# Performance work log

Hardware: AMD Instinct MI355X
Metric: run time of the kernel (lower is better)

Reference implementation:

```python
import jax, jax.numpy as jnp
import numpy as np

V = 20000          # vocab size ('ALL')
E = 512            # embedding_dim
H = 1024           # rnn_hidden_size
LD = 256           # latent_dim
NL = 2             # num_rnn_layers_dec (hidden_factor = 2, unidirectional)
B = 32
S = 256
PAD = 0
CUT0 = 30          # cutoffs = [30, 100, 1000], div_value = 4.0
TAIL_SPECS = [(30, 100, 256), (100, 1000, 64), (1000, V, 16)]  # (low, high, proj_dim)


def setup_inputs() -> dict:
    key = jax.random.key(0)
    ks = jax.random.split(key, 24)
    w = lambda k, shp: (0.02 * jax.random.normal(k, shp)).astype(jnp.float32)

    z = jax.random.normal(ks[0], (B, LD), dtype=jnp.float32)
    emb = w(ks[1], (V, E))
    l2h_w = w(ks[2], (NL * H, LD))
    l2h_b = jnp.zeros((NL * H,), jnp.float32)
    # RNN layer 0 (input E) and layer 1 (input H)
    rnn0_wih = w(ks[3], (H, E)); rnn0_whh = w(ks[4], (H, H))
    rnn0_bih = jnp.zeros((H,), jnp.float32); rnn0_bhh = jnp.zeros((H,), jnp.float32)
    rnn1_wih = w(ks[5], (H, H)); rnn1_whh = w(ks[6], (H, H))
    rnn1_bih = jnp.zeros((H,), jnp.float32); rnn1_bhh = jnp.zeros((H,), jnp.float32)
    # adaptive softmax: head = 30 shortlist + 3 cluster logits
    head_w = w(ks[7], (CUT0 + 3, H))
    tail_p0 = w(ks[8], (256, H));  tail_w0 = w(ks[9], (70, 256))
    tail_p1 = w(ks[10], (64, H));  tail_w1 = w(ks[11], (900, 64))
    tail_p2 = w(ks[12], (16, H));  tail_w2 = w(ks[13], (V - 1000, 16))

    length = jax.random.randint(ks[14], (B,), 32, S + 1)
    pos = jnp.arange(S)[None, :]
    mask = pos < length[:, None]
    inp_seq = jax.random.randint(ks[15], (B, S), 4, V)
    inp_seq = jnp.where(mask, inp_seq, PAD)
    target_seq = jax.random.randint(ks[16], (B, S), 4, V)
    target_seq = jnp.where(mask, target_seq, PAD)

    return dict(z=z, emb=emb, l2h_w=l2h_w, l2h_b=l2h_b,
                rnn0_wih=rnn0_wih, rnn0_whh=rnn0_whh, rnn0_bih=rnn0_bih, rnn0_bhh=rnn0_bhh,
                rnn1_wih=rnn1_wih, rnn1_whh=rnn1_whh, rnn1_bih=rnn1_bih, rnn1_bhh=rnn1_bhh,
                head_w=head_w, tail_p0=tail_p0, tail_w0=tail_w0, tail_p1=tail_p1,
                tail_w1=tail_w1, tail_p2=tail_p2, tail_w2=tail_w2,
                inp_seq=inp_seq, target_seq=target_seq, length=length)


def _rnn_layer(x, h0, wih, whh, bih, bhh):
    # x: [B,S,D], h0: [B,H] -> [B,S,H]  (tanh vanilla RNN)
    def step(h, xt):
        h = jnp.tanh(xt @ wih.T + bih + h @ whh.T + bhh)
        return h, h
    _, ys = jax.lax.scan(step, h0, jnp.swapaxes(x, 0, 1))
    return jnp.swapaxes(ys, 0, 1)


def _adaptive_log_prob(x, head_w, tails):
    # x: [N,H] -> full log-probs [N,V] (AdaptiveLogSoftmaxWithLoss.log_prob)
    head_lp = jax.nn.log_softmax(x @ head_w.T, axis=-1)  # [N, 33]
    parts = [head_lp[:, :CUT0]]
    for i, (p, w) in enumerate(tails):
        clp = jax.nn.log_softmax((x @ p.T) @ w.T, axis=-1)
        parts.append(clp + head_lp[:, CUT0 + i][:, None])
    return jnp.concatenate(parts, axis=1)


def reference(z, emb, l2h_w, l2h_b,
              rnn0_wih, rnn0_whh, rnn0_bih, rnn0_bhh,
              rnn1_wih, rnn1_whh, rnn1_bih, rnn1_bhh,
              head_w, tail_p0, tail_w0, tail_p1, tail_w1, tail_p2, tail_w2,
              inp_seq, target_seq, length):
    # sort inputs by descending length (hidden is NOT sorted, as in the original)
    sorted_idx = jnp.argsort(-length)
    x = emb[inp_seq[sorted_idx]]                         # [B,S,E]
    hid = z @ l2h_w.T + l2h_b                            # [B, 2H]
    hidden = hid.reshape(NL, B, H)                       # torch .view(hidden_factor, B, H)
    h1 = _rnn_layer(x, hidden[0], rnn0_wih, rnn0_whh, rnn0_bih, rnn0_bhh)
    h2 = _rnn_layer(h1, hidden[1], rnn1_wih, rnn1_whh, rnn1_bih, rnn1_bhh)
    rev = jnp.argsort(sorted_idx)
    out = h2[rev].reshape(-1, H)                         # [N,H]
    tgt = target_seq.reshape(-1)                         # [N]
    lp = _adaptive_log_prob(out, head_w,
                            [(tail_p0, tail_w0), (tail_p1, tail_w1), (tail_p2, tail_w2)])
    nll = -jnp.take_along_axis(lp, tgt[:, None], axis=1)[:, 0]
    nll = jnp.where(tgt == PAD, 0.0, nll)
    return jnp.sum(nll)
```

## Files before the change

### kernel.cpp

```cpp
#include <hip/hip_runtime.h>
#include <hip/hip_bf16.h>
#include <math.h>

#define BB 32
#define SS 256
#define EE 512
#define HH 1024
#define LDM 256
#define NROW (BB*SS)
#define NWG 64

typedef __attribute__((ext_vector_type(8))) short bf16x8;
typedef __attribute__((ext_vector_type(4))) float f32x4;
typedef unsigned long long u64;

static __device__ inline unsigned short f2bf(float f){
  unsigned u = __float_as_uint(f);
  unsigned r = (u + 0x7fffu + ((u >> 16) & 1u)) >> 16;
  return (unsigned short)r;
}
static __device__ inline unsigned short f2bf_fast(float f){
  return (unsigned short)((__float_as_uint(f) + 0x8000u) >> 16);
}
static __device__ inline bf16x8 cvt8(float4 x, float4 y){
  union { ushort s[8]; bf16x8 v; } t;
  t.s[0]=f2bf_fast(x.x); t.s[1]=f2bf_fast(x.y); t.s[2]=f2bf_fast(x.z); t.s[3]=f2bf_fast(x.w);
  t.s[4]=f2bf_fast(y.x); t.s[5]=f2bf_fast(y.y); t.s[6]=f2bf_fast(y.z); t.s[7]=f2bf_fast(y.w);
  return t.v;
}
static __device__ inline unsigned packbf(float a, float b){
  return (unsigned)f2bf(a) | ((unsigned)f2bf(b) << 16);
}

static __device__ inline float ftanh(float x){
  float e = __expf(2.f*x);
  return 1.f - 2.f/(e + 1.f);
}

#define GLD(dst, p) asm volatile("global_load_dwordx4 %0, %1, off sc0 sc1" \
                                 : "=v"(dst) : "v"(p) : "memory")

static __device__ inline bf16x8 asbf(f32x4 x){
  union { f32x4 f; bf16x8 b; } u; u.f = x; return u.b;
}

__global__ void k_sort(const int* __restrict__ length, int* __restrict__ sorted_idx){
  int b = threadIdx.x;
  if (b >= BB) return;
  int lb = length[b];
  int r = 0;
  for (int o = 0; o < BB; ++o){
    int lo = length[o];
    if (lo > lb || (lo == lb && o < b)) ++r;
  }
  sorted_idx[r] = b;
}

__global__ void k_maps(const int* __restrict__ sorted_idx,
                       const int* __restrict__ inp_seq, const int* __restrict__ tgt_seq,
                       int* __restrict__ tokmap, int* __restrict__ tgtmap){
  int bs = blockIdx.x; int t = threadIdx.x;
  int b = sorted_idx[bs];
  tokmap[bs*SS + t] = inp_seq[b*SS + t];
  tgtmap[bs*SS + t] = tgt_seq[b*SS + t];
}

__global__ __launch_bounds__(256) void k_hid(const float* __restrict__ z,
        const float* __restrict__ w, const float* __restrict__ bias,
        ushort* __restrict__ hb0){
  int id = blockIdx.x*256 + threadIdx.x;
  int b = id >> 11, c = id & 2047;
  const float4* zr = (const float4*)(z + b*LDM);
  const float4* wr = (const float4*)(w + (size_t)c*LDM);
  float a0=0,a1=0,a2=0,a3=0;
  #pragma unroll 4
  for (int k=0;k<LDM/4;k++){ float4 zz=zr[k], ww=wr[k];
    a0+=zz.x*ww.x; a1+=zz.y*ww.y; a2+=zz.z*ww.z; a3+=zz.w*ww.w; }
  float val = a0+a1+a2+a3 + bias[c];
  int layer = id >> 15, bp = (id >> 10) & 31, j = id & 1023;
  hb0[(layer<<15) + ((j>>3)<<8) + (bp<<3) + (j&7)] = f2bf(val);
}

__global__ __launch_bounds__(256) void k_gemm_bf16(
    const float* __restrict__ A, int lda, const int* __restrict__ rowmap,
    const float* __restrict__ Bm,
    const float* __restrict__ bias0, const float* __restrict__ bias1,
    float* __restrict__ C, int M, int N, int K)
{
  __shared__ ushort As[128*72];
  __shared__ ushort Bs[128*72];
  const int nt = blockIdx.x * 128, mt = blockIdx.y * 128;
  const int tid = threadIdx.x;
  const int wv = tid >> 6, ln = tid & 63;
  const int wm = wv & 1, wn = wv >> 1;
  const int lc = ln & 15, quad = ln >> 4;
  f32x4 acc[4][4] = {{{0.f,0.f,0.f,0.f}}};

  for (int s = 0; s < K; s += 64){
    __syncthreads();
    #pragma unroll
    for (int cc = 0; cc < 4; ++cc){
      int ch = tid*4 + cc;
      int r = ch >> 3, c = ch & 7;
      int ar = mt + r;
      const float* ap = A + (size_t)(rowmap ? rowmap[ar] : ar)*lda + s + c*8;
      float4 x = *(const float4*)ap, y = *(const float4*)(ap+4);
      *(bf16x8*)&As[r*72 + c*8] = cvt8(x, y);
      int br = nt + r; if (br >= N) br = N - 1;
      const float* bp = Bm + (size_t)br*K + s + c*8;
      float4 bx = *(const float4*)bp, by = *(const float4*)(bp+4);
      *(bf16x8*)&Bs[r*72 + c*8] = cvt8(bx, by);
    }
    __syncthreads();
    #pragma unroll
    for (int kq = 0; kq < 2; ++kq){
      int cq = kq*4 + quad;
      bf16x8 af[4], bfv[4];
      #pragma unroll
      for (int i=0;i<4;i++) af[i]  = *(const bf16x8*)&As[(wm*64 + i*16 + lc)*72 + cq*8];
      #pragma unroll
      for (int j=0;j<4;j++) bfv[j] = *(const bf16x8*)&Bs[(wn*64 + j*16 + lc)*72 + cq*8];
      #pragma unroll
      for (int i=0;i<4;i++)
        #pragma unroll
        for (int j=0;j<4;j++)
          acc[i][j] = __builtin_amdgcn_mfma_f32_16x16x32_bf16(af[i], bfv[j], acc[i][j], 0, 0, 0);
    }
  }
  #pragma unroll
  for (int j=0;j<4;j++){
    int col = nt + wn*64 + j*16 + lc;
    if (col < N){
      float badd = (bias0 ? bias0[col] : 0.f) + (bias1 ? bias1[col] : 0.f);
      #pragma unroll
      for (int i=0;i<4;i++){
        int row = mt + wm*64 + i*16 + quad*4;
        #pragma unroll
        for (int r=0;r<4;r++)
          C[(size_t)(row+r)*N + col] = acc[i][j][r] + badd;
      }
    }
  }
}

__global__ __launch_bounds__(256, 1) void k_rnn_fused(
    const float* __restrict__ pre0, float* __restrict__ h2out,
    const float* __restrict__ w0hh, const float* __restrict__ w1ih,
    const float* __restrict__ w1hh,
    const float* __restrict__ b1ih, const float* __restrict__ b1hh,
    const ushort* __restrict__ hb0, ushort* __restrict__ hx, int* ctr)
{
  __shared__ ushort w0F[16384], wiF[16384], whF[16384];
  __shared__ float red[4352];
  const int wg  = blockIdx.x;
  const int tid = threadIdx.x;
  const int j0  = wg * 16;

  for (int c = tid; c < 4096; c += 256){
    int rr = c >> 8, cc = (c & 255) * 4;
    int dst = ((cc >> 3)*16 + rr)*8 + (cc & 7);
    size_t srow = (size_t)(j0 + rr)*HH + cc;
    float4 w4; uint2 p;
    w4 = *(const float4*)&w0hh[srow];
    p.x = packbf(w4.x, w4.y); p.y = packbf(w4.z, w4.w);
    *(uint2*)&w0F[dst] = p;
    w4 = *(const float4*)&w1ih[srow];
    p.x = packbf(w4.x, w4.y); p.y = packbf(w4.z, w4.w);
    *(uint2*)&wiF[dst] = p;
    w4 = *(const float4*)&w1hh[srow];
    p.x = packbf(w4.x, w4.y); p.y = packbf(w4.z, w4.w);
    *(uint2*)&whF[dst] = p;
  }
  const int lane = tid & 63, wv = tid >> 6;
  const int col = lane & 15, quad = lane >> 4;
  const int ob = tid >> 3, oj = (tid << 1) & 15;

  float2 pre = *(const float2*)&pre0[((size_t)ob*SS + 0)*HH + j0 + oj];
  float2 pre2;
  pre2.x = b1ih[j0+oj]   + b1hh[j0+oj];
  pre2.y = b1ih[j0+oj+1] + b1hh[j0+oj+1];
  __syncthreads();

  for (int r = 0; r < SS; ++r){
    const u64* s1 = (const u64*)(r == 0 ? hb0 : hx + ((r-1)&1)*32768);
    const u64* s2 = (r == 0) ? (const u64*)hb0
                  : (const u64*)(r == 1 ? hb0 + 32768 : hx + (2 + (r&1))*32768);
    f32x4 a0r[8], a1r[8], c0r[8], c1r[8];
    #pragma unroll
    for (int ks = 0; ks < 8; ++ks){
      int kb = wv*32 + ks*4 + quad;
      const u64* p = s1 + (kb << 6) + (col << 1);
      GLD(a0r[ks], p);
      GLD(a1r[ks], p + 32);
    }
    if (r > 0){
      #pragma unroll
      for (int ks = 0; ks < 8; ++ks){
        int kb = wv*32 + ks*4 + quad;
        const u64* p = s2 + (kb << 6) + (col << 1);
        GLD(c0r[ks], p);
        GLD(c1r[ks], p + 32);
      }
    }
    asm volatile("s_waitcnt vmcnt(0)" ::: "memory");
    __builtin_amdgcn_sched_barrier(0);

    f32x4 accA0 = {0.f,0.f,0.f,0.f}, accA1 = {0.f,0.f,0.f,0.f};
    f32x4 accB0 = {0.f,0.f,0.f,0.f}, accB1 = {0.f,0.f,0.f,0.f};
    #pragma unroll
    for (int ks = 0; ks < 8; ++ks){
      int kb = wv*32 + ks*4 + quad;
      bf16x8 b0 = *(const bf16x8*)&w0F[(kb*16 + col)*8];
      accA0 = __builtin_amdgcn_mfma_f32_16x16x32_bf16(asbf(a0r[ks]), b0, accA0, 0, 0, 0);
      accA1 = __builtin_amdgcn_mfma_f32_16x16x32_bf16(asbf(a1r[ks]), b0, accA1, 0, 0, 0);
      bf16x8 bi = *(const bf16x8*)&wiF[(kb*16 + col)*8];
      accB0 = __builtin_amdgcn_mfma_f32_16x16x32_bf16(asbf(a0r[ks]), bi, accB0, 0, 0, 0);
      accB1 = __builtin_amdgcn_mfma_f32_16x16x32_bf16(asbf(a1r[ks]), bi, accB1, 0, 0, 0);
    }
    if (r > 0){
      #pragma unroll
      for (int ks = 0; ks < 8; ++ks){
        int kb = wv*32 + ks*4 + quad;
        bf16x8 bh = *(const bf16x8*)&whF[(kb*16 + col)*8];
        accB0 = __builtin_amdgcn_mfma_f32_16x16x32_bf16(asbf(c0r[ks]), bh, accB0, 0, 0, 0);
        accB1 = __builtin_amdgcn_mfma_f32_16x16x32_bf16(asbf(c1r[ks]), bh, accB1, 0, 0, 0);
      }
    }
    #pragma unroll
    for (int q = 0; q < 4; ++q){
      red[wv*544 + (quad*4 + q)*17 + col]             = accA0[q];
      red[wv*544 + (16 + quad*4 + q)*17 + col]        = accA1[q];
      red[2176 + wv*544 + (quad*4 + q)*17 + col]      = accB0[q];
      red[2176 + wv*544 + (16 + quad*4 + q)*17 + col] = accB1[q];
    }
    __syncthreads();

    int ro = ob*17 + oj;
    float s0 = red[ro]   + red[544 + ro]   + red[1088 + ro]   + red[1632 + ro];
    float s1v= red[ro+1] + red[544 + ro+1] + red[1088 + ro+1] + red[1632 + ro+1];
    float v0 = ftanh(pre.x + s0);
    float v1 = ftanh(pre.y + s1v);
    int k = j0 + oj;
    unsigned off = ((unsigned)(k >> 3) << 7) + ((unsigned)ob << 2) + ((unsigned)(k & 7) >> 1);
    __hip_atomic_store((unsigned*)(hx + (r&1)*32768) + off, packbf(v0, v1),
                       __ATOMIC_RELAXED, __HIP_MEMORY_SCOPE_AGENT);
    float w0v = 0.f, w1v = 0.f;
    if (r > 0){
      float s2v = red[2176+ro]   + red[2720+ro]   + red[3264+ro]   + red[3808+ro];
      float s3v = red[2176+ro+1] + red[2720+ro+1] + red[3264+ro+1] + red[3808+ro+1];
      w0v = ftanh(pre2.x + s2v);
      w1v = ftanh(pre2.y + s3v);
      __hip_atomic_store((unsigned*)(hx + (2 + ((r-1)&1))*32768) + off, packbf(w0v, w1v),
                         __ATOMIC_RELAXED, __HIP_MEMORY_SCOPE_AGENT);
    }
    asm volatile("s_waitcnt vmcnt(0)" ::: "memory");
    __syncthreads();
    if (tid == 0)
      __hip_atomic_fetch_add(ctr, 1, __ATOMIC_RELAXED, __HIP_MEMORY_SCOPE_AGENT);

    if (r > 0)
      *(float2*)&h2out[((size_t)ob*SS + (r-1))*HH + j0 + oj] = make_float2(w0v, w1v);
    int tn = (r + 1 < SS) ? r + 1 : SS - 1;
    pre = *(const float2*)&pre0[((size_t)ob*SS + tn)*HH + j0 + oj];

    if (tid == 0){
      int tv = (r + 1) * NWG;
      while (__hip_atomic_load(ctr, __ATOMIC_RELAXED, __HIP_MEMORY_SCOPE_AGENT) < tv) {}
    }
    __syncthreads();
  }

  {
    const u64* s1 = (const u64*)(hx + 32768);
    const u64* s2 = (const u64*)(hx + 2*32768);
    f32x4 a0r[8], a1r[8], c0r[8], c1r[8];
    #pragma unroll
    for (int ks = 0; ks < 8; ++ks){
      int kb = wv*32 + ks*4 + quad;
      const u64* p1 = s1 + (kb << 6) + (col << 1);
      GLD(a0r[ks], p1); GLD(a1r[ks], p1 + 32);
      const u64* p2 = s2 + (kb << 6) + (col << 1);
      GLD(c0r[ks], p2); GLD(c1r[ks], p2 + 32);
    }
    asm volatile("s_waitcnt vmcnt(0)" ::: "memory");
    __builtin_amdgcn_sched_barrier(0);
    f32x4 accB0 = {0.f,0.f,0.f,0.f}, accB1 = {0.f,0.f,0.f,0.f};
    #pragma unroll
    for (int ks = 0; ks < 8; ++ks){
      int kb = wv*32 + ks*4 + quad;
      bf16x8 bi = *(const bf16x8*)&wiF[(kb*16 + col)*8];
      accB0 = __builtin_amdgcn_mfma_f32_16x16x32_bf16(asbf(a0r[ks]), bi, accB0, 0, 0, 0);
      accB1 = __builtin_amdgcn_mfma_f32_16x16x32_bf16(asbf(a1r[ks]), bi, accB1, 0, 0, 0);
      bf16x8 bh = *(const bf16x8*)&whF[(kb*16 + col)*8];
      accB0 = __builtin_amdgcn_mfma_f32_16x16x32_bf16(asbf(c0r[ks]), bh, accB0, 0, 0, 0);
      accB1 = __builtin_amdgcn_mfma_f32_16x16x32_bf16(asbf(c1r[ks]), bh, accB1, 0, 0, 0);
    }
    #pragma unroll
    for (int q = 0; q < 4; ++q){
      red[wv*544 + (quad*4 + q)*17 + col]      = accB0[q];
      red[wv*544 + (16 + quad*4 + q)*17 + col] = accB1[q];
    }
    __syncthreads();
    int ro = ob*17 + oj;
    float s2v = red[ro]   + red[544 + ro]   + red[1088 + ro]   + red[1632 + ro];
    float s3v = red[ro+1] + red[544 + ro+1] + red[1088 + ro+1] + red[1632 + ro+1];
    *(float2*)&h2out[((size_t)ob*SS + (SS-1))*HH + j0 + oj] =
        make_float2(ftanh(pre2.x + s2v), ftanh(pre2.y + s3v));
  }
}

__global__ __launch_bounds__(256) void k_cluster(
    const float* __restrict__ proj, int Kp,
    const float* __restrict__ W, int Nc,
    float* __restrict__ stats, int ci)
{
  __shared__ float ps[4][4][256];
  int lane = threadIdx.x & 63;
  int wvl  = threadIdx.x >> 6;
  int r0 = (blockIdx.x*4 + wvl) * 4;
  for (int r=0;r<4;r++)
    for (int k=lane;k<Kp;k+=64)
      ps[wvl][r][k] = proj[(size_t)(r0+r)*Kp + k];
  __syncthreads();
  float mx[4], sm[4];
  #pragma unroll
  for (int r=0;r<4;r++){ mx[r]=-1e30f; sm[r]=0.f; }
  for (int n=lane; n<Nc; n+=64){
    const float* wr = W + (size_t)n*Kp;
    float l[4]={0.f,0.f,0.f,0.f};
    for (int k=0;k<Kp;k+=4){
      float4 w4 = *(const float4*)(wr+k);
      #pragma unroll
      for (int r=0;r<4;r++){
        l[r] += w4.x*ps[wvl][r][k] + w4.y*ps[wvl][r][k+1]
              + w4.z*ps[wvl][r][k+2] + w4.w*ps[wvl][r][k+3];
      }
    }
    #pragma unroll
    for (int r=0;r<4;r++){
      float nm = fmaxf(mx[r], l[r]);
      sm[r] = sm[r]*__expf(mx[r]-nm) + __expf(l[r]-nm);
      mx[r] = nm;
    }
  }
  #pragma unroll
  for (int r=0;r<4;r++){
    for (int off=32; off; off>>=1){
      float om = __shfl_down(mx[r], off);
      float os = __shfl_down(sm[r], off);
      float nm = fmaxf(mx[r], om);
      sm[r] = sm[r]*__expf(mx[r]-nm) + os*__expf(om-nm);
      mx[r] = nm;
    }
    if (lane==0){
      stats[(size_t)(r0+r)*6 + ci*2 + 0] = mx[r];
      stats[(size_t)(r0+r)*6 + ci*2 + 1] = sm[r];
    }
  }
}

__global__ __launch_bounds__(256) void k_tlogit(
    const int* __restrict__ tgtmap,
    const float* __restrict__ proj0, const float* __restrict__ proj1, const float* __restrict__ proj2,
    const float* __restrict__ w0, const float* __restrict__ w1, const float* __restrict__ w2,
    float* __restrict__ tlogit)
{
  int lane = threadIdx.x & 63;
  int row = (blockIdx.x * 256 + threadIdx.x) >> 6;
  int tgt = tgtmap[row];
  float acc = 0.f;
  const float* pr = nullptr; const float* wr = nullptr; int Kp = 0;
  if      (tgt >= 1000){ pr = proj2 + (size_t)row*16;  wr = w2 + (size_t)(tgt-1000)*16;  Kp=16;  }
  else if (tgt >= 100) { pr = proj1 + (size_t)row*64;  wr = w1 + (size_t)(tgt-100)*64;   Kp=64;  }
  else if (tgt >= 30)  { pr = proj0 + (size_t)row*256; wr = w0 + (size_t)(tgt-30)*256;   Kp=256; }
  for (int k=lane; k<Kp; k+=64) acc += pr[k]*wr[k];
  for (int off=32; off; off>>=1) acc += __shfl_down(acc, off);
  if (lane==0) tlogit[row] = acc;
}

__global__ __launch_bounds__(256) void k_final(
    const float* __restrict__ head, const float* __restrict__ stats,
    const float* __restrict__ tlogit, const int* __restrict__ tgtmap,
    float* __restrict__ out)
{
  int row = blockIdx.x*256 + threadIdx.x;
  int tgt = tgtmap[row];
  float nll = 0.f;
  if (tgt != 0){
    const float* hrow = head + (size_t)row*33;
    float m = hrow[0];
    #pragma unroll
    for (int i=1;i<33;i++) m = fmaxf(m, hrow[i]);
    float s = 0.f;
    #pragma unroll
    for (int i=0;i<33;i++) s += __expf(hrow[i]-m);
    float lse = __logf(s) + m;
    int ci = (tgt>=1000) ? 2 : (tgt>=100) ? 1 : (tgt>=30) ? 0 : -1;
    if (ci < 0){
      nll = lse - hrow[tgt];
    } else {
      float cm = stats[(size_t)row*6 + ci*2 + 0];
      float cs = stats[(size_t)row*6 + ci*2 + 1];
      nll = lse - hrow[30+ci] + (__logf(cs) + cm - tlogit[row]);
    }
  }
  float v = nll;
  for (int off=32; off; off>>=1) v += __shfl_down(v, off);
  __shared__ float wsum[4];
  int lane = threadIdx.x & 63, wv = threadIdx.x >> 6;
  if (lane==0) wsum[wv] = v;
  __syncthreads();
  if (threadIdx.x==0) atomicAdd(out, wsum[0]+wsum[1]+wsum[2]+wsum[3]);
}

extern "C" void kernel_launch(void* const* d_in, const int* in_sizes, int n_in,
                              void* d_out, int out_size, void* d_ws, size_t ws_size,
                              hipStream_t stream)
{
  const float* z      = (const float*)d_in[0];
  const float* emb    = (const float*)d_in[1];
  const float* l2h_w  = (const float*)d_in[2];
  const float* l2h_b  = (const float*)d_in[3];
  const float* w0ih   = (const float*)d_in[4];
  const float* w0hh   = (const float*)d_in[5];
  const float* b0ih   = (const float*)d_in[6];
  const float* b0hh   = (const float*)d_in[7];
  const float* w1ih   = (const float*)d_in[8];
  const float* w1hh   = (const float*)d_in[9];
  const float* b1ih   = (const float*)d_in[10];
  const float* b1hh   = (const float*)d_in[11];
  const float* head_w = (const float*)d_in[12];
  const float* p0     = (const float*)d_in[13];
  const float* tw0    = (const float*)d_in[14];
  const float* p1     = (const float*)d_in[15];
  const float* tw1    = (const float*)d_in[16];
  const float* p2     = (const float*)d_in[17];
  const float* tw2    = (const float*)d_in[18];
  const int* inp_seq  = (const int*)d_in[19];
  const int* tgt_seq  = (const int*)d_in[20];
  const int* length   = (const int*)d_in[21];

  float* ws   = (float*)d_ws;
  ushort* hb0 = (ushort*)ws;
  ushort* hx  = hb0 + 65536;
  float* bufA = ws + 98304;
  float* bufB = bufA + (size_t)NROW*HH;
  int*   ibuf = (int*)(bufB + (size_t)NROW*HH);
  int* sorted_idx = ibuf;
  int* tokmap = ibuf + 32;
  int* tgtmap = tokmap + NROW;
  int* flags  = tgtmap + NROW;
  float* headL = bufA;
  float* proj0 = headL + (size_t)NROW*33;
  float* proj1 = proj0 + (size_t)NROW*256;
  float* proj2 = proj1 + (size_t)NROW*64;
  float* stats = proj2 + (size_t)NROW*16;
  float* tlog  = stats + (size_t)NROW*6;

  float* outF = (float*)d_out;
  hipMemsetAsync(outF, 0, sizeof(float), stream);
  hipMemsetAsync(flags, 0, 128*sizeof(int), stream);

  k_sort<<<1, 32, 0, stream>>>(length, sorted_idx);
  k_maps<<<32, 256, 0, stream>>>(sorted_idx, inp_seq, tgt_seq, tokmap, tgtmap);
  k_hid<<<256, 256, 0, stream>>>(z, l2h_w, l2h_b, hb0);

  k_gemm_bf16<<<dim3(HH/128, NROW/128), 256, 0, stream>>>(emb, EE, tokmap, w0ih,
                                                          b0ih, b0hh, bufA, NROW, HH, EE);
  k_rnn_fused<<<NWG, 256, 0, stream>>>(bufA, bufB, w0hh, w1ih, w1hh, b1ih, b1hh,
                                       hb0, hx, flags);

  k_gemm_bf16<<<dim3(1, NROW/128), 256, 0, stream>>>(bufB, HH, nullptr, head_w,
                                                     nullptr, nullptr, headL, NROW, 33, HH);
  k_gemm_bf16<<<dim3(2, NROW/128), 256, 0, stream>>>(bufB, HH, nullptr, p0,
                                                     nullptr, nullptr, proj0, NROW, 256, HH);
  k_gemm_bf16<<<dim3(1, NROW/128), 256, 0, stream>>>(bufB, HH, nullptr, p1,
                                                     nullptr, nullptr, proj1, NROW, 64, HH);
  k_gemm_bf16<<<dim3(1, NROW/128), 256, 0, stream>>>(bufB, HH, nullptr, p2,
                                                     nullptr, nullptr, proj2, NROW, 16, HH);

  k_cluster<<<NROW/16, 256, 0, stream>>>(proj0, 256, tw0, 70,    stats, 0);
  k_cluster<<<NROW/16, 256, 0, stream>>>(proj1, 64,  tw1, 900,   stats, 1);
  k_cluster<<<NROW/16, 256, 0, stream>>>(proj2, 16,  tw2, 19000, stats, 2);
  k_tlogit<<<NROW/4, 256, 0, stream>>>(tgtmap, proj0, proj1, proj2, tw0, tw1, tw2, tlog);
  k_final<<<NROW/256, 256, 0, stream>>>(headL, stats, tlog, tgtmap, outF);
}
```

Before: 1.794 ms.

## Fuse adaptive-softmax projections into one GEMM and shard RNN barrier counters

Concatenates head and tail projection weights into a single padded 384-row matrix so one GEMM produces all head logits and cluster projections, reading the RNN output once instead of four times. Downstream cluster, tlogit and final kernels index into the combined strided buffer. The RNN per-step grid barrier now spreads arrivals over 8 padded counters, with 8 threads polling, to reduce atomic contention. This adds a small weight-copy kernel and some padding compute.

```diff
diff --git a/kernel.cpp b/kernel.cpp
--- a/kernel.cpp
+++ b/kernel.cpp
@@ -81,6 +81,21 @@
   hb0[(layer<<15) + ((j>>3)<<8) + (bp<<3) + (j&7)] = f2bf(val);
 }
 
+__global__ __launch_bounds__(256) void k_wcat(
+    const float* __restrict__ head_w, const float* __restrict__ p0,
+    const float* __restrict__ p1, const float* __restrict__ p2,
+    float* __restrict__ wcat){
+  int row = blockIdx.x; int t = threadIdx.x;
+  float4* dst = (float4*)(wcat + (size_t)row*HH);
+  const float* src;
+  if      (row < 33)  src = head_w + (size_t)row*HH;
+  else if (row < 289) src = p0 + (size_t)(row-33)*HH;
+  else if (row < 353) src = p1 + (size_t)(row-289)*HH;
+  else if (row < 369) src = p2 + (size_t)(row-353)*HH;
+  else { dst[t] = make_float4(0.f,0.f,0.f,0.f); return; }
+  dst[t] = ((const float4*)src)[t];
+}
+
 __global__ __launch_bounds__(256) void k_gemm_bf16(
     const float* __restrict__ A, int lda, const int* __restrict__ rowmap,
     const float* __restrict__ Bm,
@@ -148,13 +163,14 @@
     const float* __restrict__ w0hh, const float* __restrict__ w1ih,
     const float* __restrict__ w1hh,
     const float* __restrict__ b1ih, const float* __restrict__ b1hh,
-    const ushort* __restrict__ hb0, ushort* __restrict__ hx, int* ctr)
+    const ushort* __restrict__ hb0, ushort* __restrict__ hx, int* flags)
 {
   __shared__ ushort w0F[16384], wiF[16384], whF[16384];
   __shared__ float red[4352];
   const int wg  = blockIdx.x;
   const int tid = threadIdx.x;
   const int j0  = wg * 16;
+  int* ctr = flags + (wg & 7) * 32;
 
   for (int c = tid; c < 4096; c += 256){
     int rr = c >> 8, cc = (c & 255) * 4;
@@ -263,9 +279,10 @@
     int tn = (r + 1 < SS) ? r + 1 : SS - 1;
     pre = *(const float2*)&pre0[((size_t)ob*SS + tn)*HH + j0 + oj];
 
-    if (tid == 0){
-      int tv = (r + 1) * NWG;
-      while (__hip_atomic_load(ctr, __ATOMIC_RELAXED, __HIP_MEMORY_SCOPE_AGENT) < tv) {}
+    if (tid < 8){
+      int tv = 8 * (r + 1);
+      while (__hip_atomic_load(flags + tid*32, __ATOMIC_RELAXED,
+                               __HIP_MEMORY_SCOPE_AGENT) < tv) {}
     }
     __syncthreads();
   }
@@ -310,7 +327,7 @@
 }
 
 __global__ __launch_bounds__(256) void k_cluster(
-    const float* __restrict__ proj, int Kp,
+    const float* __restrict__ proj, int ld, int Kp,
     const float* __restrict__ W, int Nc,
     float* __restrict__ stats, int ci)
 {
@@ -320,7 +337,7 @@
   int r0 = (blockIdx.x*4 + wvl) * 4;
   for (int r=0;r<4;r++)
     for (int k=lane;k<Kp;k+=64)
-      ps[wvl][r][k] = proj[(size_t)(r0+r)*Kp + k];
+      ps[wvl][r][k] = proj[(size_t)(r0+r)*ld + k];
   __syncthreads();
   float mx[4], sm[4];
   #pragma unroll
@@ -360,8 +377,7 @@
 }
 
 __global__ __launch_bounds__(256) void k_tlogit(
-    const int* __restrict__ tgtmap,
-    const float* __restrict__ proj0, const float* __restrict__ proj1, const float* __restrict__ proj2,
+    const int* __restrict__ tgtmap, const float* __restrict__ combo,
     const float* __restrict__ w0, const float* __restrict__ w1, const float* __restrict__ w2,
     float* __restrict__ tlogit)
 {
@@ -370,16 +386,17 @@
   int tgt = tgtmap[row];
   float acc = 0.f;
   const float* pr = nullptr; const float* wr = nullptr; int Kp = 0;
-  if      (tgt >= 1000){ pr = proj2 + (size_t)row*16;  wr = w2 + (size_t)(tgt-1000)*16;  Kp=16;  }
-  else if (tgt >= 100) { pr = proj1 + (size_t)row*64;  wr = w1 + (size_t)(tgt-100)*64;   Kp=64;  }
-  else if (tgt >= 30)  { pr = proj0 + (size_t)row*256; wr = w0 + (size_t)(tgt-30)*256;   Kp=256; }
+  const float* crow = combo + (size_t)row*384;
+  if      (tgt >= 1000){ pr = crow + 353; wr = w2 + (size_t)(tgt-1000)*16;  Kp=16;  }
+  else if (tgt >= 100) { pr = crow + 289; wr = w1 + (size_t)(tgt-100)*64;   Kp=64;  }
+  else if (tgt >= 30)  { pr = crow + 33;  wr = w0 + (size_t)(tgt-30)*256;   Kp=256; }
   for (int k=lane; k<Kp; k+=64) acc += pr[k]*wr[k];
   for (int off=32; off; off>>=1) acc += __shfl_down(acc, off);
   if (lane==0) tlogit[row] = acc;
 }
 
 __global__ __launch_bounds__(256) void k_final(
-    const float* __restrict__ head, const float* __restrict__ stats,
+    const float* __restrict__ combo, const float* __restrict__ stats,
     const float* __restrict__ tlogit, const int* __restrict__ tgtmap,
     float* __restrict__ out)
 {
@@ -387,7 +404,7 @@
   int tgt = tgtmap[row];
   float nll = 0.f;
   if (tgt != 0){
-    const float* hrow = head + (size_t)row*33;
+    const float* hrow = combo + (size_t)row*384;
     float m = hrow[0];
     #pragma unroll
     for (int i=1;i<33;i++) m = fmaxf(m, hrow[i]);
@@ -450,16 +467,14 @@
   int* tokmap = ibuf + 32;
   int* tgtmap = tokmap + NROW;
   int* flags  = tgtmap + NROW;
-  float* headL = bufA;
-  float* proj0 = headL + (size_t)NROW*33;
-  float* proj1 = proj0 + (size_t)NROW*256;
-  float* proj2 = proj1 + (size_t)NROW*64;
-  float* stats = proj2 + (size_t)NROW*16;
+  float* combo = bufA;
+  float* stats = bufA + (size_t)NROW*384;
   float* tlog  = stats + (size_t)NROW*6;
+  float* wcat  = tlog + NROW;
 
   float* outF = (float*)d_out;
   hipMemsetAsync(outF, 0, sizeof(float), stream);
-  hipMemsetAsync(flags, 0, 128*sizeof(int), stream);
+  hipMemsetAsync(flags, 0, 512*sizeof(int), stream);
 
   k_sort<<<1, 32, 0, stream>>>(length, sorted_idx);
   k_maps<<<32, 256, 0, stream>>>(sorted_idx, inp_seq, tgt_seq, tokmap, tgtmap);
@@ -470,18 +485,13 @@
   k_rnn_fused<<<NWG, 256, 0, stream>>>(bufA, bufB, w0hh, w1ih, w1hh, b1ih, b1hh,
                                        hb0, hx, flags);
 
-  k_gemm_bf16<<<dim3(1, NROW/128), 256, 0, stream>>>(bufB, HH, nullptr, head_w,
-                                                     nullptr, nullptr, headL, NROW, 33, HH);
-  k_gemm_bf16<<<dim3(2, NROW/128), 256, 0, stream>>>(bufB, HH, nullptr, p0,
-                                                     nullptr, nullptr, proj0, NROW, 256, HH);
-  k_gemm_bf16<<<dim3(1, NROW/128), 256, 0, stream>>>(bufB, HH, nullptr, p1,
-                                                     nullptr, nullptr, proj1, NROW, 64, HH);
-  k_gemm_bf16<<<dim3(1, NROW/128), 256, 0, stream>>>(bufB, HH, nullptr, p2,
-                                                     nullptr, nullptr, proj2, NROW, 16, HH);
-
-  k_cluster<<<NROW/16, 256, 0, stream>>>(proj0, 256, tw0, 70,    stats, 0);
-  k_cluster<<<NROW/16, 256, 0, stream>>>(proj1, 64,  tw1, 900,   stats, 1);
-  k_cluster<<<NROW/16, 256, 0, stream>>>(proj2, 16,  tw2, 19000, stats, 2);
-  k_tlogit<<<NROW/4, 256, 0, stream>>>(tgtmap, proj0, proj1, proj2, tw0, tw1, tw2, tlog);
-  k_final<<<NROW/256, 256, 0, stream>>>(headL, stats, tlog, tgtmap, outF);
-}
+  k_wcat<<<384, 256, 0, stream>>>(head_w, p0, p1, p2, wcat);
+  k_gemm_bf16<<<dim3(3, NROW/128), 256, 0, stream>>>(bufB, HH, nullptr, wcat,
+                                                     nullptr, nullptr, combo, NROW, 384, HH);
+
+  k_cluster<<<NROW/16, 256, 0, stream>>>(combo + 33,  384, 256, tw0, 70,    stats, 0);
+  k_cluster<<<NROW/16, 256, 0, stream>>>(combo + 289, 384, 64,  tw1, 900,   stats, 1);
+  k_cluster<<<NROW/16, 256, 0, stream>>>(combo + 353, 384, 16,  tw2, 19000, stats, 2);
+  k_tlogit<<<NROW/4, 256, 0, stream>>>(tgtmap, combo, tw0, tw1, tw2, tlog);
+  k_final<<<NROW/256, 256, 0, stream>>>(combo, stats, tlog, tgtmap, outF);
+}
```

Measured after the change: 1.578 ms. -12.1%, faster.
